# Kernel tuning notes

Hardware: AMD Instinct MI355X
Metric: run time of the kernel (lower is better)

Reference implementation:

```python
import jax, jax.numpy as jnp
import numpy as np

# DeformConv hyperparameters (from init_kwargs)
KH, KW = 3, 3
STRIDE, PAD, DIL = 1, 1, 1
GROUPS, DG = 1, 1  # groups=1, deformable_groups=1
B, C, H, W = 4, 64, 128, 128
O = 64
HO = (H + 2 * PAD - (DIL * (KH - 1) + 1)) // STRIDE + 1  # 128
WO = (W + 2 * PAD - (DIL * (KW - 1) + 1)) // STRIDE + 1  # 128


def setup_inputs() -> dict:
    key = jax.random.key(0)
    k1, k2, k3, k4 = jax.random.split(key, 4)
    x = jax.random.normal(k1, (B, C, H, W), dtype=jnp.float32)
    # offset channels: dg * K * 2, ordered (y, x) per kernel tap (DCNv1 CUDA layout)
    offset = jax.random.normal(k2, (B, 2 * DG * KH * KW, HO, WO), dtype=jnp.float32)
    fan_in = C * KH * KW
    weight = jax.random.normal(k3, (O, C // GROUPS, KH, KW), dtype=jnp.float32) / np.sqrt(fan_in)
    bias = jax.random.normal(k4, (O,), dtype=jnp.float32) * 0.01
    return {"x": x, "offset": offset, "weight": weight, "bias": bias}


def _deform_sample(x, offset):
    """Bilinear-sample x at deformed kernel tap locations.
    Returns [B, C, K, HO, WO] where K = KH*KW."""
    K = KH * KW
    Cg = C // DG
    # offset -> [B, DG, K, 2, HO, WO]; channel layout: dg*2*K, pairs (y, x)
    off = offset.reshape(B, DG, K, 2, HO, WO)
    off_y, off_x = off[:, :, :, 0], off[:, :, :, 1]  # [B, DG, K, HO, WO]

    ki = (jnp.arange(K) // KW).astype(jnp.float32)  # kernel row
    kj = (jnp.arange(K) % KW).astype(jnp.float32)   # kernel col
    base_h = (jnp.arange(HO) * STRIDE - PAD).astype(jnp.float32)
    base_w = (jnp.arange(WO) * STRIDE - PAD).astype(jnp.float32)

    # sampling positions [B, DG, K, HO, WO]
    py = off_y + (ki * DIL)[None, None, :, None, None] + base_h[None, None, None, :, None]
    px = off_x + (kj * DIL)[None, None, :, None, None] + base_w[None, None, None, None, :]

    y0f = jnp.floor(py)
    x0f = jnp.floor(px)
    ly = py - y0f
    lx = px - x0f
    hy = 1.0 - ly
    hx = 1.0 - lx
    y0 = y0f.astype(jnp.int32)
    x0 = x0f.astype(jnp.int32)
    y1 = y0 + 1
    x1 = x0 + 1

    flat = x.reshape(B, DG, Cg, H * W)

    def gather(yi, xi, wgt):
        valid = (yi >= 0) & (yi < H) & (xi >= 0) & (xi < W)
        idx = jnp.clip(yi, 0, H - 1) * W + jnp.clip(xi, 0, W - 1)
        idx = idx.reshape(B, DG, 1, K * HO * WO)
        v = jnp.take_along_axis(flat, idx, axis=-1).reshape(B, DG, Cg, K, HO, WO)
        return v * (wgt * valid.astype(wgt.dtype))[:, :, None]

    val = (gather(y0, x0, hy * hx) + gather(y0, x1, hy * lx)
           + gather(y1, x0, ly * hx) + gather(y1, x1, ly * lx))
    return val.reshape(B, C, K, HO, WO)


def reference(x, offset, weight, bias):
    sampled = _deform_sample(x, offset)              # [B, C, K, HO, WO]
    w = weight.reshape(O, C, KH * KW)                # groups = 1
    out = jnp.einsum('bckhw,ock->bohw', sampled, w)  # im2col + GEMM
    return out + bias[None, :, None, None]
```

## Files before the change

### kernel.cpp

```cpp
#include <hip/hip_runtime.h>
#include <hip/hip_fp16.h>


#define B_  4
#define C_  64
#define H_  128
#define W_  128
#define O_  64
#define HO_ 128
#define WO_ 128
#define NCHUNK 8
#define NGW 12
#define KSTEPS 3
#define NT_ 32
#define NTASK (9 * NT_)
#define SG  10
#define SBUF (SG * NT_ * 8)
#define TR  16
#define TC  48
#define TSLOTS (TR * TC)

typedef _Float16 half8 __attribute__((ext_vector_type(8)));
typedef __attribute__((ext_vector_type(4))) float f32x4;

union H8 { float4 v; __half2 h2[4]; half8 v8; };

__global__ __launch_bounds__(256)
void prep(const float* __restrict__ x, const float* __restrict__ w,
          __half* __restrict__ xt, __half* __restrict__ wt) {
    const int tid = threadIdx.x;
    if (blockIdx.x < 2048) {
        int t = blockIdx.x * 256 + tid;
        int xc = t & 127;
        int y  = (t >> 7) & 127;
        int ch = (t >> 14) & 7;
        int b  = t >> 17;
        const float* xp = x + (((size_t)(b * C_ + ch * 8) * H_) + y) * W_ + xc;
        union { __half h[8]; float4 v; } pk;
#pragma unroll
        for (int e = 0; e < 8; ++e) pk.h[e] = __float2half_rn(xp[e * H_ * W_]);
        *(float4*)(xt + (size_t)t * 8) = pk.v;
    } else {
        int t = (blockIdx.x - 2048) * 256 + tid;
        if (t >= NCHUNK * NGW * O_) return;
        int o  = t & 63;
        int g  = (t >> 6) % NGW;
        int ch = (t >> 6) / NGW;
        union { __half h[8]; float4 v; } pk;
#pragma unroll
        for (int e = 0; e < 8; ++e)
            pk.h[e] = (g < 9) ? __float2half_rn(w[(o * C_ + ch * 8 + e) * 9 + g])
                              : __half(0.0f);
        *(float4*)(wt + (size_t)t * 8) = pk.v;
    }
}

__global__ __launch_bounds__(256, 4)
void dcn_mfma(const __half* __restrict__ xt, const float* __restrict__ off,
              const __half* __restrict__ wt, const float* __restrict__ bias,
              float* __restrict__ out) {
    __shared__ __align__(16) _Float16 sS[2 * SBUF];
    __shared__ __align__(16) _Float16 sT[TSLOTS * 8];

    const int tid = threadIdx.x;
    const int bid = blockIdx.x;
    const int w4  = bid & 3;
    const int ho  = (bid >> 2) & (HO_ - 1);
    const int b   = bid >> 9;
    const int woB = w4 * NT_;
    const int yb  = ho - 7;
    const int xb  = woB - 8;

    int ty0_[2], ty1_[2], tx_[2], fb_[2];
    __half2 ua2_[2], ub2_[2], va2_[2], vb2_[2];
#pragma unroll
    for (int r = 0; r < 2; ++r) {
        int task = tid + r * 256;
        int tk = (task < NTASK) ? task : 0;
        int k  = tk >> 5;
        int wo = (tk & (NT_ - 1)) + woB;
        int ki = k / 3, kj = k - 3 * ki;
        float oy = off[(((b * 18) + 2 * k    ) * HO_ + ho) * WO_ + wo];
        float ox = off[(((b * 18) + 2 * k + 1) * HO_ + ho) * WO_ + wo];
        float py = (float)(ho - 1 + ki) + oy;
        float px = (float)(wo - 1 + kj) + ox;
        float y0f = floorf(py), x0f = floorf(px);
        int   y0 = (int)y0f,   x0 = (int)x0f;
        float ly = py - y0f,   lx = px - x0f;
        float hy = 1.f - ly,   hx = 1.f - lx;
        int y1 = y0 + 1, x1 = x0 + 1;
        float vy0 = (y0 >= 0 && y0 < H_) ? 1.f : 0.f;
        float vy1 = (y1 >= 0 && y1 < H_) ? 1.f : 0.f;
        float vx0 = (x0 >= 0 && x0 < W_) ? 1.f : 0.f;
        float vx1 = (x1 >= 0 && x1 < W_) ? 1.f : 0.f;
        int cy0 = min(max(y0, 0), H_ - 1), cy1 = min(max(y1, 0), H_ - 1);
        int cx0 = min(max(x0, 0), W_ - 1), cx1 = min(max(x1, 0), W_ - 1);
        int ax  = min(max(x0, 0), W_ - 2);
        float w00 = hy * hx * vy0 * vx0;
        float w01 = hy * lx * vy0 * vx1;
        float w10 = ly * hx * vy1 * vx0;
        float w11 = ly * lx * vy1 * vx1;
        float s0 = (cx0 != ax) ? 1.f : 0.f;
        float s1 = (cx1 != ax) ? 1.f : 0.f;
        ty0_[r] = cy0 - yb;
        ty1_[r] = cy1 - yb;
        tx_[r]  = ax - xb;
        fb_[r]  = ((unsigned)ty0_[r] > (unsigned)(TR - 1)) |
                  ((unsigned)ty1_[r] > (unsigned)(TR - 1)) |
                  ((unsigned)tx_[r]  > (unsigned)(TC - 2));
        ua2_[r] = __float2half2_rn(w00 * (1.f - s0) + w01 * (1.f - s1));
        ub2_[r] = __float2half2_rn(w00 * s0 + w01 * s1);
        va2_[r] = __float2half2_rn(w10 * (1.f - s0) + w11 * (1.f - s1));
        vb2_[r] = __float2half2_rn(w10 * s0 + w11 * s1);
    }

    int gofs[3];
#pragma unroll
    for (int j = 0; j < 3; ++j) {
        int s  = tid + j * 256;
        int rr = s / TC, cc = s - rr * TC;
        int yc = min(max(yb + rr, 0), H_ - 1);
        int xc = min(max(xb + cc, 0), W_ - 1);
        gofs[j] = yc * W_ + xc;
    }

    if (tid < 128) {
        ((unsigned int*)&sS[9 * NT_ * 8])[tid]        = 0u;
        ((unsigned int*)&sS[SBUF + 9 * NT_ * 8])[tid] = 0u;
    }

    float4 pf0, pf1, pf2;
    auto issue = [&](int ch) {
        const float4* xc = (const float4*)(xt + ((size_t)(b * NCHUNK + ch)) * (H_ * W_ * 8));
        pf0 = xc[gofs[0]];
        pf1 = xc[gofs[1]];
        pf2 = xc[gofs[2]];
    };

    auto sample = [&](int ch) {
        _Float16* buf = sS + (ch & 1) * SBUF;
        const float4* xcg = (const float4*)(xt + ((size_t)(b * NCHUNK + ch)) * (H_ * W_ * 8));
        const float4* tl  = (const float4*)sT;
#pragma unroll
        for (int r = 0; r < 2; ++r) {
            int task = tid + r * 256;
            if (task < NTASK) {
                int k  = task >> 5;
                int wo = task & (NT_ - 1);
                H8 q00, q01, q10, q11;
                if (!fb_[r]) {
                    int a0 = ty0_[r] * TC + tx_[r];
                    int a1 = ty1_[r] * TC + tx_[r];
                    q00.v = tl[a0];  q01.v = tl[a0 + 1];
                    q10.v = tl[a1];  q11.v = tl[a1 + 1];
                } else {
                    int a0 = (ty0_[r] + yb) * W_ + (tx_[r] + xb);
                    int a1 = (ty1_[r] + yb) * W_ + (tx_[r] + xb);
                    q00.v = xcg[a0]; q01.v = xcg[a0 + 1];
                    q10.v = xcg[a1]; q11.v = xcg[a1 + 1];
                }
                H8 s;
#pragma unroll
                for (int j = 0; j < 4; ++j) {
                    __half2 t0 = __hmul2(ua2_[r], q00.h2[j]);
                    t0 = __hfma2(ub2_[r], q01.h2[j], t0);
                    t0 = __hfma2(va2_[r], q10.h2[j], t0);
                    t0 = __hfma2(vb2_[r], q11.h2[j], t0);
                    s.h2[j] = t0;
                }
                *(half8*)&buf[(k * NT_ + wo) * 8] = s.v8;
            }
        }
    };

    const int lane = tid & 63;
    const int wv   = tid >> 6;
    const int ow   = wv & 1;
    const int nw   = wv >> 1;
    const int quad = lane >> 4;
    const int l15  = lane & 15;

    f32x4 acc[2];
    acc[0] = (f32x4){0.f, 0.f, 0.f, 0.f};
    acc[1] = (f32x4){0.f, 0.f, 0.f, 0.f};

    auto mfma_chunk = [&](int ch) {
        const __half*   wc  = wt + (size_t)(ch * NGW) * O_ * 8;
        const _Float16* buf = sS + (ch & 1) * SBUF;
#pragma unroll
        for (int ks = 0; ks < KSTEPS; ++ks) {
            int g  = ks * 4 + quad;
            int gb = (g < 9) ? g : 9;
            half8 bfr = *(const half8*)&buf[(gb * NT_ + nw * 16 + l15) * 8];
#pragma unroll
            for (int ot = 0; ot < 2; ++ot) {
                half8 afr = *(const half8*)(wc + (size_t)(g * O_ + ow * 32 + ot * 16 + l15) * 8);
                acc[ot] = __builtin_amdgcn_mfma_f32_16x16x32_f16(afr, bfr, acc[ot], 0, 0, 0);
            }
        }
    };

    issue(0);
    for (int ch = 0; ch < NCHUNK; ++ch) {
        float4* tw = (float4*)sT;
        tw[tid]       = pf0;
        tw[tid + 256] = pf1;
        tw[tid + 512] = pf2;
        __syncthreads();
        if (ch + 1 < NCHUNK) issue(ch + 1);
        sample(ch);
        if (ch > 0) mfma_chunk(ch - 1);
        __syncthreads();
    }
    mfma_chunk(NCHUNK - 1);

#pragma unroll
    for (int ot = 0; ot < 2; ++ot) {
        int wo = woB + nw * 16 + l15;
#pragma unroll
        for (int rg = 0; rg < 4; ++rg) {
            int o = ow * 32 + ot * 16 + quad * 4 + rg;
            out[(((size_t)(b * O_ + o)) * HO_ + ho) * WO_ + wo] = acc[ot][rg] + bias[o];
        }
    }
}

extern "C" void kernel_launch(void* const* d_in, const int* in_sizes, int n_in,
                              void* d_out, int out_size, void* d_ws, size_t ws_size,
                              hipStream_t stream) {
    const float* x    = (const float*)d_in[0];
    const float* off  = (const float*)d_in[1];
    const float* w    = (const float*)d_in[2];
    const float* bias = (const float*)d_in[3];
    float* out = (float*)d_out;

    __half* wt = (__half*)d_ws;
    __half* xt = (__half*)((char*)d_ws + 262144);

    hipLaunchKernelGGL(prep, dim3(2048 + 24), dim3(256), 0, stream, x, w, xt, wt);
    hipLaunchKernelGGL(dcn_mfma, dim3(B_ * HO_ * (WO_ / NT_)), dim3(256), 0, stream,
                       xt, off, wt, bias, out);
}
```

Baseline: 101.1 us.

## Fuse fp16 input conversion into main kernel, drop transposed x staging buffer

Removes the prep pass that converts x to a channel-interleaved fp16 layout and instead loads fp32 x directly in the main kernel, converting each tile to half while staging it into shared memory. The goal is to avoid writing and re-reading a full fp16 copy of the input through global memory. In exchange, each tile load now issues eight strided scalar fp32 loads instead of one 16-byte vector load. The register prefetch that overlapped the next chunk's load with sampling is gone, so global load latency is exposed on every chunk.

```diff
diff --git a/kernel.cpp b/kernel.cpp
--- a/kernel.cpp
+++ b/kernel.cpp
@@ -9,6 +9,7 @@
 #define O_  64
 #define HO_ 128
 #define WO_ 128
+#define HW_ (H_ * W_)
 #define NCHUNK 8
 #define NGW 12
 #define KSTEPS 3
@@ -23,40 +24,25 @@
 typedef _Float16 half8 __attribute__((ext_vector_type(8)));
 typedef __attribute__((ext_vector_type(4))) float f32x4;
 
-union H8 { float4 v; __half2 h2[4]; half8 v8; };
+union H8 { float4 v; __half2 h2[4]; half8 v8; __half h[8]; };
 
 __global__ __launch_bounds__(256)
-void prep(const float* __restrict__ x, const float* __restrict__ w,
-          __half* __restrict__ xt, __half* __restrict__ wt) {
-    const int tid = threadIdx.x;
-    if (blockIdx.x < 2048) {
-        int t = blockIdx.x * 256 + tid;
-        int xc = t & 127;
-        int y  = (t >> 7) & 127;
-        int ch = (t >> 14) & 7;
-        int b  = t >> 17;
-        const float* xp = x + (((size_t)(b * C_ + ch * 8) * H_) + y) * W_ + xc;
-        union { __half h[8]; float4 v; } pk;
-#pragma unroll
-        for (int e = 0; e < 8; ++e) pk.h[e] = __float2half_rn(xp[e * H_ * W_]);
-        *(float4*)(xt + (size_t)t * 8) = pk.v;
-    } else {
-        int t = (blockIdx.x - 2048) * 256 + tid;
-        if (t >= NCHUNK * NGW * O_) return;
-        int o  = t & 63;
-        int g  = (t >> 6) % NGW;
-        int ch = (t >> 6) / NGW;
-        union { __half h[8]; float4 v; } pk;
-#pragma unroll
-        for (int e = 0; e < 8; ++e)
-            pk.h[e] = (g < 9) ? __float2half_rn(w[(o * C_ + ch * 8 + e) * 9 + g])
-                              : __half(0.0f);
-        *(float4*)(wt + (size_t)t * 8) = pk.v;
-    }
+void prep(const float* __restrict__ w, __half* __restrict__ wt) {
+    int t = blockIdx.x * 256 + threadIdx.x;
+    if (t >= NCHUNK * NGW * O_) return;
+    int o  = t & 63;
+    int g  = (t >> 6) % NGW;
+    int ch = (t >> 6) / NGW;
+    union { __half h[8]; float4 v; } pk;
+#pragma unroll
+    for (int e = 0; e < 8; ++e)
+        pk.h[e] = (g < 9) ? __float2half_rn(w[(o * C_ + ch * 8 + e) * 9 + g])
+                          : __half(0.0f);
+    *(float4*)(wt + (size_t)t * 8) = pk.v;
 }
 
 __global__ __launch_bounds__(256, 4)
-void dcn_mfma(const __half* __restrict__ xt, const float* __restrict__ off,
+void dcn_mfma(const float* __restrict__ x, const float* __restrict__ off,
               const __half* __restrict__ wt, const float* __restrict__ bias,
               float* __restrict__ out) {
     __shared__ __align__(16) _Float16 sS[2 * SBUF];
@@ -68,8 +54,8 @@
     const int ho  = (bid >> 2) & (HO_ - 1);
     const int b   = bid >> 9;
     const int woB = w4 * NT_;
-    const int yb  = ho - 7;
-    const int xb  = woB - 8;
+    const int yorg = ho - 7;
+    const int xorg = woB - 8;
 
     int ty0_[2], ty1_[2], tx_[2], fb_[2];
     __half2 ua2_[2], ub2_[2], va2_[2], vb2_[2];
@@ -102,9 +88,9 @@
         float w11 = ly * lx * vy1 * vx1;
         float s0 = (cx0 != ax) ? 1.f : 0.f;
         float s1 = (cx1 != ax) ? 1.f : 0.f;
-        ty0_[r] = cy0 - yb;
-        ty1_[r] = cy1 - yb;
-        tx_[r]  = ax - xb;
+        ty0_[r] = cy0 - yorg;
+        ty1_[r] = cy1 - yorg;
+        tx_[r]  = ax - xorg;
         fb_[r]  = ((unsigned)ty0_[r] > (unsigned)(TR - 1)) |
                   ((unsigned)ty1_[r] > (unsigned)(TR - 1)) |
                   ((unsigned)tx_[r]  > (unsigned)(TC - 2));
@@ -119,8 +105,8 @@
     for (int j = 0; j < 3; ++j) {
         int s  = tid + j * 256;
         int rr = s / TC, cc = s - rr * TC;
-        int yc = min(max(yb + rr, 0), H_ - 1);
-        int xc = min(max(xb + cc, 0), W_ - 1);
+        int yc = min(max(yorg + rr, 0), H_ - 1);
+        int xc = min(max(xorg + cc, 0), W_ - 1);
         gofs[j] = yc * W_ + xc;
     }
 
@@ -129,44 +115,61 @@
         ((unsigned int*)&sS[SBUF + 9 * NT_ * 8])[tid] = 0u;
     }
 
-    float4 pf0, pf1, pf2;
-    auto issue = [&](int ch) {
-        const float4* xc = (const float4*)(xt + ((size_t)(b * NCHUNK + ch)) * (H_ * W_ * 8));
-        pf0 = xc[gofs[0]];
-        pf1 = xc[gofs[1]];
-        pf2 = xc[gofs[2]];
+    auto stage = [&](int ch) {
+        const float* xb = x + ((size_t)(b * C_ + ch * 8)) * HW_;
+        float4* tw = (float4*)sT;
+#pragma unroll 1
+        for (int j = 0; j < 3; ++j) {
+            const int g = gofs[j];
+            float v[8];
+#pragma unroll
+            for (int e = 0; e < 8; ++e) v[e] = xb[e * HW_ + g];
+            H8 pk;
+#pragma unroll
+            for (int e = 0; e < 8; ++e) pk.h[e] = __float2half_rn(v[e]);
+            tw[tid + j * 256] = pk.v;
+        }
     };
 
     auto sample = [&](int ch) {
         _Float16* buf = sS + (ch & 1) * SBUF;
-        const float4* xcg = (const float4*)(xt + ((size_t)(b * NCHUNK + ch)) * (H_ * W_ * 8));
-        const float4* tl  = (const float4*)sT;
+        const float4* tl = (const float4*)sT;
 #pragma unroll
         for (int r = 0; r < 2; ++r) {
             int task = tid + r * 256;
             if (task < NTASK) {
                 int k  = task >> 5;
                 int wo = task & (NT_ - 1);
-                H8 q00, q01, q10, q11;
+                H8 s;
                 if (!fb_[r]) {
                     int a0 = ty0_[r] * TC + tx_[r];
                     int a1 = ty1_[r] * TC + tx_[r];
+                    H8 q00, q01, q10, q11;
                     q00.v = tl[a0];  q01.v = tl[a0 + 1];
                     q10.v = tl[a1];  q11.v = tl[a1 + 1];
+#pragma unroll
+                    for (int j = 0; j < 4; ++j) {
+                        __half2 t0 = __hmul2(ua2_[r], q00.h2[j]);
+                        t0 = __hfma2(ub2_[r], q01.h2[j], t0);
+                        t0 = __hfma2(va2_[r], q10.h2[j], t0);
+                        t0 = __hfma2(vb2_[r], q11.h2[j], t0);
+                        s.h2[j] = t0;
+                    }
                 } else {
-                    int a0 = (ty0_[r] + yb) * W_ + (tx_[r] + xb);
-                    int a1 = (ty1_[r] + yb) * W_ + (tx_[r] + xb);
-                    q00.v = xcg[a0]; q01.v = xcg[a0 + 1];
-                    q10.v = xcg[a1]; q11.v = xcg[a1 + 1];
-                }
-                H8 s;
-#pragma unroll
-                for (int j = 0; j < 4; ++j) {
-                    __half2 t0 = __hmul2(ua2_[r], q00.h2[j]);
-                    t0 = __hfma2(ub2_[r], q01.h2[j], t0);
-                    t0 = __hfma2(va2_[r], q10.h2[j], t0);
-                    t0 = __hfma2(vb2_[r], q11.h2[j], t0);
-                    s.h2[j] = t0;
+                    const float* xb = x + ((size_t)(b * C_ + ch * 8)) * HW_;
+                    int a0 = (ty0_[r] + yorg) * W_ + (tx_[r] + xorg);
+                    int a1 = (ty1_[r] + yorg) * W_ + (tx_[r] + xorg);
+                    float ua = __half2float(__low2half(ua2_[r]));
+                    float ub = __half2float(__low2half(ub2_[r]));
+                    float va = __half2float(__low2half(va2_[r]));
+                    float vb = __half2float(__low2half(vb2_[r]));
+#pragma unroll
+                    for (int e = 0; e < 8; ++e) {
+                        const float* xe = xb + e * HW_;
+                        float sv = ua * xe[a0] + ub * xe[a0 + 1]
+                                 + va * xe[a1] + vb * xe[a1 + 1];
+                        s.h[e] = __float2half_rn(sv);
+                    }
                 }
                 *(half8*)&buf[(k * NT_ + wo) * 8] = s.v8;
             }
@@ -200,14 +203,9 @@
         }
     };
 
-    issue(0);
     for (int ch = 0; ch < NCHUNK; ++ch) {
-        float4* tw = (float4*)sT;
-        tw[tid]       = pf0;
-        tw[tid + 256] = pf1;
-        tw[tid + 512] = pf2;
+        stage(ch);
         __syncthreads();
-        if (ch + 1 < NCHUNK) issue(ch + 1);
         sample(ch);
         if (ch > 0) mfma_chunk(ch - 1);
         __syncthreads();
@@ -235,9 +233,8 @@
     float* out = (float*)d_out;
 
     __half* wt = (__half*)d_ws;
-    __half* xt = (__half*)((char*)d_ws + 262144);
-
-    hipLaunchKernelGGL(prep, dim3(2048 + 24), dim3(256), 0, stream, x, w, xt, wt);
+
+    hipLaunchKernelGGL(prep, dim3(24), dim3(256), 0, stream, w, wt);
     hipLaunchKernelGGL(dcn_mfma, dim3(B_ * HO_ * (WO_ / NT_)), dim3(256), 0, stream,
-                       xt, off, wt, bias, out);
+                       x, off, wt, bias, out);
 }
```

Measured after the change: 121.4 us. 1.2x slower.
